# Kernel optimization log

Hardware: AMD Instinct MI355X
Metric: run time of the kernel (lower is better)

The kernel has to match this reference:

```python
import jax, jax.numpy as jnp
import numpy as np

EMBED_DIM = 1024
NUM_HEADS = 16
HEAD_DIM = EMBED_DIM // NUM_HEADS


def setup_inputs() -> dict:
    key = jax.random.key(0)
    k_x, k_wqkv, k_bqkv, k_wo, k_bo = jax.random.split(key, 5)
    B, T, C = 4, 2048, EMBED_DIM
    # PyTorch Linear default init scale ~ 1/sqrt(fan_in); use small normals
    s = 1.0 / np.sqrt(C)
    return {
        "x": jax.random.normal(k_x, (B, T, C), dtype=jnp.float32),
        "w_qkv": jax.random.normal(k_wqkv, (C, 3 * C), dtype=jnp.float32) * s,
        "b_qkv": jax.random.normal(k_bqkv, (3 * C,), dtype=jnp.float32) * s,
        "w_out": jax.random.normal(k_wo, (C, C), dtype=jnp.float32) * s,
        "b_out": jax.random.normal(k_bo, (C,), dtype=jnp.float32) * s,
    }


def reference(x, w_qkv, b_qkv, w_out, b_out):
    B, T, C = x.shape
    H, D = NUM_HEADS, HEAD_DIM
    qkv = x @ w_qkv + b_qkv                      # (B, T, 3C)
    q, k, v = jnp.split(qkv, 3, axis=-1)
    # (B, H, T, D)
    q = q.reshape(B, T, H, D).transpose(0, 2, 1, 3)
    k = k.reshape(B, T, H, D).transpose(0, 2, 1, 3)
    v = v.reshape(B, T, H, D).transpose(0, 2, 1, 3)
    scores = jnp.einsum("bhqd,bhkd->bhqk", q, k) / jnp.sqrt(jnp.float32(D))
    causal = jnp.tril(jnp.ones((T, T), dtype=bool))  # (T, T)
    scores = jnp.where(causal[None, None, :, :], scores, -jnp.inf)
    attn = jax.nn.softmax(scores, axis=-1)
    out = jnp.einsum("bhqk,bhkd->bhqd", attn, v)  # (B, H, T, D)
    out = out.transpose(0, 2, 1, 3).reshape(B, T, C)
    return out @ w_out + b_out
```

## Files before the change

### kernel.cpp

```cpp
#include <hip/hip_runtime.h>
#include <hip/hip_bf16.h>

#define B_  4
#define T_  2048
#define C_  1024
#define H_  16
#define D_  64
#define BH_ (B_*H_)

typedef float  f32x4  __attribute__((ext_vector_type(4)));
typedef __bf16 bf16x8 __attribute__((ext_vector_type(8)));
typedef __bf16 bf16x2 __attribute__((ext_vector_type(2)));

static __device__ __forceinline__ ushort f2bf(float f) {
    union { float f; unsigned u; } x; x.f = f;
    unsigned r = ((x.u >> 16) & 1u) + 0x7fffu;
    return (ushort)((x.u + r) >> 16);
}

static __device__ __forceinline__ uint packbf(float a, float b) {
    bf16x2 v = { (__bf16)a, (__bf16)b };
    return __builtin_bit_cast(uint, v);
}

static __device__ __forceinline__ void gload_lds16(const void* g, void* l) {
    __builtin_amdgcn_global_load_lds(
        (const __attribute__((address_space(1))) unsigned int*)g,
        (__attribute__((address_space(3))) unsigned int*)l, 16, 0, 0);
}

template<int N> static __device__ __forceinline__ void waitcnt_vm() {
    if constexpr (N == 0) asm volatile("s_waitcnt vmcnt(0)" ::: "memory");
    else if constexpr (N == 3) asm volatile("s_waitcnt vmcnt(3)" ::: "memory");
    else if constexpr (N == 4) asm volatile("s_waitcnt vmcnt(4)" ::: "memory");
    else static_assert(N == 0 || N == 3 || N == 4);
    __builtin_amdgcn_sched_barrier(0);
}
static __device__ __forceinline__ void lgkm0() {
    asm volatile("s_waitcnt lgkmcnt(0)" ::: "memory");
    __builtin_amdgcn_sched_barrier(0);
}

__global__ void cvt_kernel(const float* __restrict__ in, ushort* __restrict__ out, int n) {
    int i = (blockIdx.x * blockDim.x + threadIdx.x) * 4;
    if (i < n) {
        float4 v = *(const float4*)(in + i);
        ushort4 o;
        o.x = f2bf(v.x); o.y = f2bf(v.y); o.z = f2bf(v.z); o.w = f2bf(v.w);
        *(ushort4*)(out + i) = o;
    }
}

__global__ void transpose_cvt_kernel(const float* __restrict__ in, ushort* __restrict__ out,
                                     int K, int N) {
    __shared__ float tile[32][33];
    int k0 = blockIdx.y * 32, n0 = blockIdx.x * 32;
    int tx = threadIdx.x & 31, ty = threadIdx.x >> 5;
    #pragma unroll
    for (int r = 0; r < 32; r += 8)
        tile[ty + r][tx] = in[(size_t)(k0 + ty + r) * N + n0 + tx];
    __syncthreads();
    #pragma unroll
    for (int r = 0; r < 32; r += 8)
        out[(size_t)(n0 + ty + r) * K + k0 + tx] = f2bf(tile[tx][ty + r]);
}

__global__ void transpose_v_kernel(const ushort* __restrict__ v, ushort* __restrict__ vt) {
    __shared__ ushort tile[64][66];
    int bh = blockIdx.x >> 5;
    int t0 = (blockIdx.x & 31) * 64;
    const ushort* src = v  + ((size_t)bh * T_ + t0) * D_;
    ushort*       dst = vt + (size_t)bh * D_ * T_ + t0;
    int tx = threadIdx.x & 63, ty = threadIdx.x >> 6;
    #pragma unroll
    for (int r = 0; r < 64; r += 4)
        tile[ty + r][tx] = src[(size_t)(ty + r) * D_ + tx];
    __syncthreads();
    #pragma unroll
    for (int r = 0; r < 64; r += 4)
        dst[(size_t)(ty + r) * T_ + tx] = tile[tx][ty + r];
}

template<int NFR, bool QKV>
__global__ __launch_bounds__(512, 2) void gemm_hk(
    const ushort* __restrict__ A,
    const ushort* __restrict__ Bt,
    const float*  __restrict__ bias,
    void* __restrict__ outp)
{
    constexpr int NT   = 16;
    constexpr int BN   = NFR * 64;
    constexpr int ABUF = 32768;
    constexpr int BBUF = BN * 128;
    constexpr int LB   = (NFR == 4) ? 2 : 1;
    constexpr int PK   = 2 + LB;
    __shared__ __align__(16) char lds[2 * ABUF + 2 * BBUF];
    char* ldsB = lds + 2 * ABUF;

    const int m0 = blockIdx.y * 256, n0 = blockIdx.x * BN;
    const int tid = threadIdx.x, lane = tid & 63;
    const int wv = tid >> 6, wm = wv >> 2, wn = wv & 3;
    const int lr = lane & 15, lh = lane >> 4;

    const int sc = (tid & 3) ^ ((tid >> 2) & 3);
    const ushort* aA = A  + (size_t)(m0 + (tid >> 2)) * 1024 + sc * 8;
    const ushort* aB = Bt + (size_t)(n0 + (tid >> 2)) * 1024 + sc * 8;

    const int cxor = (lh ^ (lr & 3)) * 16;
    const int arow = (wm * 128 + lr) * 64 + cxor;
    const int brow = (wn * (NFR * 16) + lr) * 64 + cxor;

    f32x4 acc[8][NFR] = {};

    auto stage_a = [&](int buf, int t, int kh) {
        #pragma unroll
        for (int p = 0; p < 2; ++p)
            gload_lds16(aA + (size_t)p * 131072 + t * 64 + kh * 32,
                        lds + buf * ABUF + kh * 16384 + p * 8192 + tid * 16);
    };
    auto stage_b = [&](int buf, int t, int kh) {
        #pragma unroll
        for (int p = 0; p < LB; ++p)
            gload_lds16(aB + (size_t)p * 131072 + t * 64 + kh * 32,
                        ldsB + buf * BBUF + kh * (BBUF / 2) + p * 8192 + tid * 16);
    };
    auto read_a = [&](bf16x8 (&af)[8], int buf, int kh) {
        const char* base = lds + buf * ABUF + kh * 16384 + arow;
        #pragma unroll
        for (int mi = 0; mi < 8; ++mi) af[mi] = *(const bf16x8*)(base + mi * 1024);
    };
    auto read_b = [&](bf16x8& b0, bf16x8& b1, int buf, int kh, int nh) {
        const char* base = ldsB + buf * BBUF + kh * (BBUF / 2) + brow + nh * 2048;
        b0 = *(const bf16x8*)(base);
        b1 = *(const bf16x8*)(base + 1024);
    };

#define MFMA2(NI, BB0, BB1)                                                          \
    do {                                                                             \
        __builtin_amdgcn_s_setprio(1);                                               \
        _Pragma("unroll")                                                            \
        for (int mi = 0; mi < 8; ++mi) {                                             \
            acc[mi][NI]     = __builtin_amdgcn_mfma_f32_16x16x32_bf16(af[mi], BB0,   \
                                                     acc[mi][NI], 0, 0, 0);          \
            acc[mi][NI + 1] = __builtin_amdgcn_mfma_f32_16x16x32_bf16(af[mi], BB1,   \
                                                     acc[mi][NI + 1], 0, 0, 0);      \
        }                                                                            \
        __builtin_amdgcn_s_setprio(0);                                               \
    } while (0)

    stage_a(0, 0, 0); stage_b(0, 0, 0);
    stage_a(0, 0, 1); stage_b(0, 0, 1);
    waitcnt_vm<PK>();
    __builtin_amdgcn_s_barrier();

    for (int t = 0; t < NT; ++t) {
        const int cur = t & 1, nxt = cur ^ 1;
        const bool pf = (t + 1 < NT);
        bf16x8 af[8], b0, b1;
        if constexpr (NFR == 4) {
            read_a(af, cur, 0); read_b(b0, b1, cur, 0, 0);
            if (pf) stage_a(nxt, t + 1, 0);
            __builtin_amdgcn_s_barrier();
            lgkm0();
            MFMA2(0, b0, b1);
            read_b(b0, b1, cur, 0, 1);
            if (pf) stage_b(nxt, t + 1, 0);
            if (t < NT - 1) waitcnt_vm<4>(); else waitcnt_vm<0>();
            __builtin_amdgcn_s_barrier();
            lgkm0();
            MFMA2(2, b0, b1);
            read_a(af, cur, 1); read_b(b0, b1, cur, 1, 0);
            if (pf) stage_a(nxt, t + 1, 1);
            __builtin_amdgcn_s_barrier();
            lgkm0();
            MFMA2(0, b0, b1);
            read_b(b0, b1, cur, 1, 1);
            if (pf) stage_b(nxt, t + 1, 1);
            if (t < NT - 1) waitcnt_vm<4>();
            __builtin_amdgcn_s_barrier();
            lgkm0();
            MFMA2(2, b0, b1);
        } else {
            read_a(af, cur, 0); read_b(b0, b1, cur, 0, 0);
            if (pf) { stage_a(nxt, t + 1, 0); stage_b(nxt, t + 1, 0); }
            if (t < NT - 1) waitcnt_vm<3>(); else waitcnt_vm<0>();
            __builtin_amdgcn_s_barrier();
            lgkm0();
            MFMA2(0, b0, b1);
            read_a(af, cur, 1); read_b(b0, b1, cur, 1, 0);
            if (pf) { stage_a(nxt, t + 1, 1); stage_b(nxt, t + 1, 1); }
            if (t < NT - 1) waitcnt_vm<3>();
            __builtin_amdgcn_s_barrier();
            lgkm0();
            MFMA2(0, b0, b1);
        }
    }
#undef MFMA2

    #pragma unroll
    for (int mi = 0; mi < 8; ++mi) {
        #pragma unroll
        for (int ni = 0; ni < NFR; ++ni) {
            int col = n0 + wn * (NFR * 16) + ni * 16 + lr;
            float bv = bias[col];
            if constexpr (QKV) {
                ushort* qkv = (ushort*)outp;
                int which = col >> 10;
                int h = (col & 1023) >> 6;
                int d = col & 63;
                #pragma unroll
                for (int r = 0; r < 4; ++r) {
                    int row = m0 + wm * 128 + mi * 16 + lh * 4 + r;
                    int b = row >> 11, tt = row & 2047;
                    float v = acc[mi][ni][r] + bv;
                    if (which == 0) v *= 0.18033688011112042f;
                    qkv[(size_t)which * (BH_ * T_ * D_) +
                        (((size_t)(b * H_ + h)) * T_ + tt) * D_ + d] = f2bf(v);
                }
            } else {
                float* Cout = (float*)outp;
                #pragma unroll
                for (int r = 0; r < 4; ++r) {
                    int row = m0 + wm * 128 + mi * 16 + lh * 4 + r;
                    Cout[(size_t)row * C_ + col] = acc[mi][ni][r] + bv;
                }
            }
        }
    }
}

__global__ __launch_bounds__(256, 4) void flash_kernel(
    const ushort* __restrict__ qb,
    const ushort* __restrict__ kb,
    const ushort* __restrict__ vt,
    ushort* __restrict__ ob)
{
    __shared__ __align__(16) ushort sK[2][64 * 64];
    __shared__ __align__(16) ushort sV[2][64 * 64];
    __shared__ __align__(16) ushort sP[4][16 * 64];
    const int bh  = blockIdx.x >> 4;
    const int pr  = blockIdx.x & 15;
    const int qtA = pr, qtB = 31 - pr;
    const int lane = threadIdx.x & 63, wv = threadIdx.x >> 6;
    const int lr = lane & 15, lh = lane >> 4;

    const ushort* qrowA = qb + ((size_t)bh * T_ + qtA * 64 + wv * 16 + lr) * D_;
    const ushort* qrowB = qb + ((size_t)bh * T_ + qtB * 64 + wv * 16 + lr) * D_;
    bf16x8 qfA0 = *(const bf16x8*)(qrowA + lh * 8);
    bf16x8 qfA1 = *(const bf16x8*)(qrowA + 32 + lh * 8);
    bf16x8 qfB0 = *(const bf16x8*)(qrowB + lh * 8);
    bf16x8 qfB1 = *(const bf16x8*)(qrowB + 32 + lh * 8);

    const int srow = lane >> 3;
    const int scol = ((lane & 7) ^ srow) * 8;
    const ushort* kbase = kb + (size_t)bh * T_ * D_;
    const ushort* vbase = vt + (size_t)bh * D_ * T_;

    const int sw   = (lr & 7) << 4;
    const int off0 = (16 * lh) ^ sw;
    const int off1 = (64 + 16 * lh) ^ sw;

    f32x4 oA[4] = {}, oB[4] = {};
    float mA = -1e30f, lA = 0.f, mB = -1e30f, lB = 0.f;

    auto redmax = [&](float x) {
        x = fmaxf(x, __int_as_float(__builtin_amdgcn_ds_swizzle(__float_as_int(x), 0x401F)));
        x = fmaxf(x, __shfl_xor(x, 32, 64));
        return x;
    };
    auto redsum = [&](float x) {
        x += __int_as_float(__builtin_amdgcn_ds_swizzle(__float_as_int(x), 0x401F));
        x += __shfl_xor(x, 32, 64);
        return x;
    };

    auto tile = [&](f32x4 (&o)[4], float& mrow, float& lsum,
                    const bf16x8& q0f, const bf16x8& q1f,
                    const char* K0, const char* V0, bool diag) {
        f32x4 s[4];
        __builtin_amdgcn_s_setprio(1);
        #pragma unroll
        for (int nt = 0; nt < 4; ++nt) {
            const char* krow = K0 + (nt * 16 + lr) * 128;
            bf16x8 k0 = *(const bf16x8*)(krow + off0);
            bf16x8 k1 = *(const bf16x8*)(krow + off1);
            f32x4 a = {0.f, 0.f, 0.f, 0.f};
            a = __builtin_amdgcn_mfma_f32_16x16x32_bf16(k0, q0f, a, 0, 0, 0);
            a = __builtin_amdgcn_mfma_f32_16x16x32_bf16(k1, q1f, a, 0, 0, 0);
            s[nt] = a;
        }
        __builtin_amdgcn_s_setprio(0);
        if (diag) {
            #pragma unroll
            for (int nt = 0; nt < 4; ++nt)
                #pragma unroll
                for (int r = 0; r < 4; ++r)
                    if (nt * 16 + lh * 4 + r > wv * 16 + lr) s[nt][r] = -INFINITY;
        }

        float pmax = fmaxf(fmaxf(fmaxf(s[0][0], s[0][1]), fmaxf(s[0][2], s[0][3])),
                           fmaxf(fmaxf(s[1][0], s[1][1]), fmaxf(s[1][2], s[1][3])));
        pmax = fmaxf(pmax, fmaxf(fmaxf(fmaxf(s[2][0], s[2][1]), fmaxf(s[2][2], s[2][3])),
                                 fmaxf(fmaxf(s[3][0], s[3][1]), fmaxf(s[3][2], s[3][3]))));
        pmax = redmax(pmax);

        if (__any(pmax > mrow + 8.f)) {
            float mnew = fmaxf(mrow, pmax);
            float al = __builtin_exp2f(mrow - mnew);
            lsum *= al;
            #pragma unroll
            for (int r = 0; r < 4; ++r) {
                float ar = __shfl(al, lh * 20 + r, 64);
                o[0][r] *= ar; o[1][r] *= ar; o[2][r] *= ar; o[3][r] *= ar;
            }
            mrow = mnew;
        }

        float rsum = 0.f;
        uint pk[8];
        #pragma unroll
        for (int nt = 0; nt < 4; ++nt) {
            float p0 = __builtin_exp2f(s[nt][0] - mrow);
            float p1 = __builtin_exp2f(s[nt][1] - mrow);
            float p2 = __builtin_exp2f(s[nt][2] - mrow);
            float p3 = __builtin_exp2f(s[nt][3] - mrow);
            rsum += (p0 + p1) + (p2 + p3);
            pk[nt * 2]     = packbf(p0, p1);
            pk[nt * 2 + 1] = packbf(p2, p3);
        }
        lsum += redsum(rsum);

        char* P = (char*)sP[wv];
        {
            char* prow = P + lr * 128;
            #pragma unroll
            for (int nt = 0; nt < 4; ++nt) {
                uint2 w; w.x = pk[nt * 2]; w.y = pk[nt * 2 + 1];
                *(uint2*)(prow + ((32 * nt + 8 * lh) ^ sw)) = w;
            }
        }
        asm volatile("" ::: "memory");
        bf16x8 pf0 = *(const bf16x8*)(P + lr * 128 + off0);
        bf16x8 pf1 = *(const bf16x8*)(P + lr * 128 + off1);

        __builtin_amdgcn_s_setprio(1);
        #pragma unroll
        for (int dt = 0; dt < 4; ++dt) {
            const char* vrow = V0 + (dt * 16 + lr) * 128;
            bf16x8 v0 = *(const bf16x8*)(vrow + off0);
            bf16x8 v1 = *(const bf16x8*)(vrow + off1);
            o[dt] = __builtin_amdgcn_mfma_f32_16x16x32_bf16(pf0, v0, o[dt], 0, 0, 0);
            o[dt] = __builtin_amdgcn_mfma_f32_16x16x32_bf16(pf1, v1, o[dt], 0, 0, 0);
        }
        __builtin_amdgcn_s_setprio(0);
    };

    #pragma unroll
    for (int i = 0; i < 2; ++i) {
        int j = i * 4 + wv;
        gload_lds16(kbase + (size_t)(j * 8 + srow) * D_ + scol, &sK[0][j * 512]);
        gload_lds16(vbase + (size_t)(j * 8 + srow) * T_ + scol, &sV[0][j * 512]);
    }
    __syncthreads();

    for (int kt = 0; kt <= qtB; ++kt) {
        const int cur = kt & 1;
        if (kt < qtB) {
            const int nb = cur ^ 1;
            #pragma unroll
            for (int i = 0; i < 2; ++i) {
                int j = i * 4 + wv;
                gload_lds16(kbase + (size_t)((kt + 1) * 64 + j * 8 + srow) * D_ + scol, &sK[nb][j * 512]);
                gload_lds16(vbase + (size_t)(j * 8 + srow) * T_ + (kt + 1) * 64 + scol, &sV[nb][j * 512]);
            }
        }
        const char* K0 = (const char*)sK[cur];
        const char* V0 = (const char*)sV[cur];
        if (kt <= qtA) tile(oA, mA, lA, qfA0, qfA1, K0, V0, kt == qtA);
        tile(oB, mB, lB, qfB0, qfB1, K0, V0, kt == qtB);
        __syncthreads();
    }

    const int b = bh >> 4, h = bh & 15;
    auto writeout = [&](f32x4 (&o)[4], float lsum, int q0) {
        float inv = 1.f / lsum;
        #pragma unroll
        for (int r = 0; r < 4; ++r) {
            float ir = __shfl(inv, lh * 20 + r, 64);
            int q = q0 + lh * 4 + r;
            #pragma unroll
            for (int dt = 0; dt < 4; ++dt)
                ob[((size_t)b * T_ + q) * C_ + h * 64 + dt * 16 + lr] = f2bf(o[dt][r] * ir);
        }
    };
    writeout(oA, lA, qtA * 64 + wv * 16);
    writeout(oB, lB, qtB * 64 + wv * 16);
}

extern "C" void kernel_launch(void* const* d_in, const int* in_sizes, int n_in,
                              void* d_out, int out_size, void* d_ws, size_t ws_size,
                              hipStream_t stream) {
    const float* x     = (const float*)d_in[0];
    const float* w_qkv = (const float*)d_in[1];
    const float* b_qkv = (const float*)d_in[2];
    const float* w_out = (const float*)d_in[3];
    const float* b_out = (const float*)d_in[4];
    float* out = (float*)d_out;

    char* ws = (char*)d_ws;
    ushort* xb     = (ushort*)(ws + 0);
    ushort* wqkvT  = (ushort*)(ws + 16777216);
    ushort* woutT  = (ushort*)(ws + 23068672);
    ushort* qkv    = (ushort*)(ws + 25165824);
    ushort* vT     = (ushort*)(ws + 75497472);
    ushort* attn   = xb;
    ushort* qb = qkv;
    ushort* kb = qkv + (size_t)BH_ * T_ * D_;
    ushort* vb = qkv + (size_t)2 * BH_ * T_ * D_;

    const int nx = B_ * T_ * C_;
    cvt_kernel<<<nx / 4 / 256, 256, 0, stream>>>(x, xb, nx);
    transpose_cvt_kernel<<<dim3(3 * C_ / 32, C_ / 32), 256, 0, stream>>>(w_qkv, wqkvT, C_, 3 * C_);
    transpose_cvt_kernel<<<dim3(C_ / 32, C_ / 32), 256, 0, stream>>>(w_out, woutT, C_, C_);
    gemm_hk<4, true><<<dim3(3 * C_ / 256, B_ * T_ / 256), 512, 0, stream>>>(xb, wqkvT, b_qkv, qkv);
    transpose_v_kernel<<<BH_ * (T_ / 64), 256, 0, stream>>>(vb, vT);
    flash_kernel<<<BH_ * 16, 256, 0, stream>>>(qb, kb, vT, attn);
    gemm_hk<2, false><<<dim3(C_ / 128, B_ * T_ / 256), 512, 0, stream>>>(attn, woutT, b_out, out);
}
```

Baseline: 205.2 us.

## Store QKV in natural row-major layout and interleave A/B tiles in flash loop

The QKV GEMM epilogue now writes bf16 results row-major as (B*T, 3072) instead of scattering into a per-head (BH, T, D) layout, and it applies the Q scale as a per-block constant. The V transpose and flash kernel read Q and K directly from that layout with a 3072-element row stride. The flash kernel also splits its tile routine into QK, mask, softmax, P-write and PV stages, and issues both QK MFMA groups before either softmax so the two query tiles can overlap. This aims to get more coalesced epilogue stores and more MFMA/ALU overlap, at the cost of strided K/Q loads and higher register pressure.

```diff
diff --git a/kernel.cpp b/kernel.cpp
--- a/kernel.cpp
+++ b/kernel.cpp
@@ -65,16 +65,17 @@
         out[(size_t)(n0 + ty + r) * K + k0 + tx] = f2bf(tile[tx][ty + r]);
 }
 
-__global__ void transpose_v_kernel(const ushort* __restrict__ v, ushort* __restrict__ vt) {
+__global__ void transpose_v_kernel(const ushort* __restrict__ qkvN, ushort* __restrict__ vt) {
     __shared__ ushort tile[64][66];
     int bh = blockIdx.x >> 5;
     int t0 = (blockIdx.x & 31) * 64;
-    const ushort* src = v  + ((size_t)bh * T_ + t0) * D_;
+    int b = bh >> 4, h = bh & 15;
+    const ushort* src = qkvN + (size_t)(b * T_ + t0) * 3072 + 2048 + h * 64;
     ushort*       dst = vt + (size_t)bh * D_ * T_ + t0;
     int tx = threadIdx.x & 63, ty = threadIdx.x >> 6;
     #pragma unroll
     for (int r = 0; r < 64; r += 4)
-        tile[ty + r][tx] = src[(size_t)(ty + r) * D_ + tx];
+        tile[ty + r][tx] = src[(size_t)(ty + r) * 3072 + tx];
     __syncthreads();
     #pragma unroll
     for (int r = 0; r < 64; r += 4)
@@ -197,28 +198,30 @@
     }
 #undef MFMA2
 
-    #pragma unroll
-    for (int mi = 0; mi < 8; ++mi) {
-        #pragma unroll
-        for (int ni = 0; ni < NFR; ++ni) {
-            int col = n0 + wn * (NFR * 16) + ni * 16 + lr;
-            float bv = bias[col];
-            if constexpr (QKV) {
-                ushort* qkv = (ushort*)outp;
-                int which = col >> 10;
-                int h = (col & 1023) >> 6;
-                int d = col & 63;
+    if constexpr (QKV) {
+        ushort* qkvN = (ushort*)outp;
+        const float qs = (n0 < 1024) ? 0.18033688011112042f : 1.f;
+        #pragma unroll
+        for (int mi = 0; mi < 8; ++mi) {
+            #pragma unroll
+            for (int ni = 0; ni < NFR; ++ni) {
+                int col = n0 + wn * (NFR * 16) + ni * 16 + lr;
+                float bv = bias[col];
                 #pragma unroll
                 for (int r = 0; r < 4; ++r) {
                     int row = m0 + wm * 128 + mi * 16 + lh * 4 + r;
-                    int b = row >> 11, tt = row & 2047;
-                    float v = acc[mi][ni][r] + bv;
-                    if (which == 0) v *= 0.18033688011112042f;
-                    qkv[(size_t)which * (BH_ * T_ * D_) +
-                        (((size_t)(b * H_ + h)) * T_ + tt) * D_ + d] = f2bf(v);
+                    qkvN[(size_t)row * 3072 + col] = f2bf((acc[mi][ni][r] + bv) * qs);
                 }
-            } else {
-                float* Cout = (float*)outp;
+            }
+        }
+    } else {
+        float* Cout = (float*)outp;
+        #pragma unroll
+        for (int mi = 0; mi < 8; ++mi) {
+            #pragma unroll
+            for (int ni = 0; ni < NFR; ++ni) {
+                int col = n0 + wn * (NFR * 16) + ni * 16 + lr;
+                float bv = bias[col];
                 #pragma unroll
                 for (int r = 0; r < 4; ++r) {
                     int row = m0 + wm * 128 + mi * 16 + lh * 4 + r;
@@ -230,8 +233,7 @@
 }
 
 __global__ __launch_bounds__(256, 4) void flash_kernel(
-    const ushort* __restrict__ qb,
-    const ushort* __restrict__ kb,
+    const ushort* __restrict__ qkvN,
     const ushort* __restrict__ vt,
     ushort* __restrict__ ob)
 {
@@ -243,17 +245,20 @@
     const int qtA = pr, qtB = 31 - pr;
     const int lane = threadIdx.x & 63, wv = threadIdx.x >> 6;
     const int lr = lane & 15, lh = lane >> 4;
-
-    const ushort* qrowA = qb + ((size_t)bh * T_ + qtA * 64 + wv * 16 + lr) * D_;
-    const ushort* qrowB = qb + ((size_t)bh * T_ + qtB * 64 + wv * 16 + lr) * D_;
-    bf16x8 qfA0 = *(const bf16x8*)(qrowA + lh * 8);
-    bf16x8 qfA1 = *(const bf16x8*)(qrowA + 32 + lh * 8);
-    bf16x8 qfB0 = *(const bf16x8*)(qrowB + lh * 8);
-    bf16x8 qfB1 = *(const bf16x8*)(qrowB + 32 + lh * 8);
+    const int b = bh >> 4, h = bh & 15;
+
+    const ushort* qN = qkvN + (size_t)b * T_ * 3072 + h * 64;
+    const ushort* kN = qN + 1024;
+
+    const ushort* qrA = qN + (size_t)(qtA * 64 + wv * 16 + lr) * 3072;
+    const ushort* qrB = qN + (size_t)(qtB * 64 + wv * 16 + lr) * 3072;
+    bf16x8 qfA0 = *(const bf16x8*)(qrA + lh * 8);
+    bf16x8 qfA1 = *(const bf16x8*)(qrA + 32 + lh * 8);
+    bf16x8 qfB0 = *(const bf16x8*)(qrB + lh * 8);
+    bf16x8 qfB1 = *(const bf16x8*)(qrB + 32 + lh * 8);
 
     const int srow = lane >> 3;
     const int scol = ((lane & 7) ^ srow) * 8;
-    const ushort* kbase = kb + (size_t)bh * T_ * D_;
     const ushort* vbase = vt + (size_t)bh * D_ * T_;
 
     const int sw   = (lr & 7) << 4;
@@ -274,10 +279,7 @@
         return x;
     };
 
-    auto tile = [&](f32x4 (&o)[4], float& mrow, float& lsum,
-                    const bf16x8& q0f, const bf16x8& q1f,
-                    const char* K0, const char* V0, bool diag) {
-        f32x4 s[4];
+    auto qk = [&](f32x4 (&s)[4], const bf16x8& q0f, const bf16x8& q1f, const char* K0) {
         __builtin_amdgcn_s_setprio(1);
         #pragma unroll
         for (int nt = 0; nt < 4; ++nt) {
@@ -290,20 +292,20 @@
             s[nt] = a;
         }
         __builtin_amdgcn_s_setprio(0);
-        if (diag) {
-            #pragma unroll
-            for (int nt = 0; nt < 4; ++nt)
-                #pragma unroll
-                for (int r = 0; r < 4; ++r)
-                    if (nt * 16 + lh * 4 + r > wv * 16 + lr) s[nt][r] = -INFINITY;
-        }
-
+    };
+    auto mask = [&](f32x4 (&s)[4]) {
+        #pragma unroll
+        for (int nt = 0; nt < 4; ++nt)
+            #pragma unroll
+            for (int r = 0; r < 4; ++r)
+                if (nt * 16 + lh * 4 + r > wv * 16 + lr) s[nt][r] = -INFINITY;
+    };
+    auto smax = [&](f32x4 (&s)[4], float& mrow, float& lsum, f32x4 (&o)[4], uint (&pk)[8]) {
         float pmax = fmaxf(fmaxf(fmaxf(s[0][0], s[0][1]), fmaxf(s[0][2], s[0][3])),
                            fmaxf(fmaxf(s[1][0], s[1][1]), fmaxf(s[1][2], s[1][3])));
         pmax = fmaxf(pmax, fmaxf(fmaxf(fmaxf(s[2][0], s[2][1]), fmaxf(s[2][2], s[2][3])),
                                  fmaxf(fmaxf(s[3][0], s[3][1]), fmaxf(s[3][2], s[3][3]))));
         pmax = redmax(pmax);
-
         if (__any(pmax > mrow + 8.f)) {
             float mnew = fmaxf(mrow, pmax);
             float al = __builtin_exp2f(mrow - mnew);
@@ -315,9 +317,7 @@
             }
             mrow = mnew;
         }
-
         float rsum = 0.f;
-        uint pk[8];
         #pragma unroll
         for (int nt = 0; nt < 4; ++nt) {
             float p0 = __builtin_exp2f(s[nt][0] - mrow);
@@ -329,20 +329,18 @@
             pk[nt * 2 + 1] = packbf(p2, p3);
         }
         lsum += redsum(rsum);
-
-        char* P = (char*)sP[wv];
-        {
-            char* prow = P + lr * 128;
-            #pragma unroll
-            for (int nt = 0; nt < 4; ++nt) {
-                uint2 w; w.x = pk[nt * 2]; w.y = pk[nt * 2 + 1];
-                *(uint2*)(prow + ((32 * nt + 8 * lh) ^ sw)) = w;
-            }
-        }
-        asm volatile("" ::: "memory");
-        bf16x8 pf0 = *(const bf16x8*)(P + lr * 128 + off0);
-        bf16x8 pf1 = *(const bf16x8*)(P + lr * 128 + off1);
-
+    };
+    auto pwrite = [&](uint (&pk)[8]) {
+        char* prow = (char*)sP[wv] + lr * 128;
+        #pragma unroll
+        for (int nt = 0; nt < 4; ++nt) {
+            uint2 w; w.x = pk[nt * 2]; w.y = pk[nt * 2 + 1];
+            *(uint2*)(prow + ((32 * nt + 8 * lh) ^ sw)) = w;
+        }
+    };
+    auto pv = [&](f32x4 (&o)[4], const char* V0) {
+        bf16x8 pf0 = *(const bf16x8*)((char*)sP[wv] + lr * 128 + off0);
+        bf16x8 pf1 = *(const bf16x8*)((char*)sP[wv] + lr * 128 + off1);
         __builtin_amdgcn_s_setprio(1);
         #pragma unroll
         for (int dt = 0; dt < 4; ++dt) {
@@ -358,7 +356,7 @@
     #pragma unroll
     for (int i = 0; i < 2; ++i) {
         int j = i * 4 + wv;
-        gload_lds16(kbase + (size_t)(j * 8 + srow) * D_ + scol, &sK[0][j * 512]);
+        gload_lds16(kN + (size_t)(j * 8 + srow) * 3072 + scol, &sK[0][j * 512]);
         gload_lds16(vbase + (size_t)(j * 8 + srow) * T_ + scol, &sV[0][j * 512]);
     }
     __syncthreads();
@@ -370,18 +368,41 @@
             #pragma unroll
             for (int i = 0; i < 2; ++i) {
                 int j = i * 4 + wv;
-                gload_lds16(kbase + (size_t)((kt + 1) * 64 + j * 8 + srow) * D_ + scol, &sK[nb][j * 512]);
+                gload_lds16(kN + (size_t)((kt + 1) * 64 + j * 8 + srow) * 3072 + scol, &sK[nb][j * 512]);
                 gload_lds16(vbase + (size_t)(j * 8 + srow) * T_ + (kt + 1) * 64 + scol, &sV[nb][j * 512]);
             }
         }
+        const bool doA = kt <= qtA;
         const char* K0 = (const char*)sK[cur];
         const char* V0 = (const char*)sV[cur];
-        if (kt <= qtA) tile(oA, mA, lA, qfA0, qfA1, K0, V0, kt == qtA);
-        tile(oB, mB, lB, qfB0, qfB1, K0, V0, kt == qtB);
+
+        f32x4 sb[4];
+        uint pk[8];
+        if (doA) {
+            f32x4 sa[4];
+            qk(sb, qfB0, qfB1, K0);
+            qk(sa, qfA0, qfA1, K0);
+            if (kt == qtB) mask(sb);
+            if (kt == qtA) mask(sa);
+            smax(sa, mA, lA, oA, pk);
+            pwrite(pk);
+            asm volatile("" ::: "memory");
+            pv(oA, V0);
+            smax(sb, mB, lB, oB, pk);
+            pwrite(pk);
+            asm volatile("" ::: "memory");
+            pv(oB, V0);
+        } else {
+            qk(sb, qfB0, qfB1, K0);
+            if (kt == qtB) mask(sb);
+            smax(sb, mB, lB, oB, pk);
+            pwrite(pk);
+            asm volatile("" ::: "memory");
+            pv(oB, V0);
+        }
         __syncthreads();
     }
 
-    const int b = bh >> 4, h = bh & 15;
     auto writeout = [&](f32x4 (&o)[4], float lsum, int q0) {
         float inv = 1.f / lsum;
         #pragma unroll
@@ -411,19 +432,16 @@
     ushort* xb     = (ushort*)(ws + 0);
     ushort* wqkvT  = (ushort*)(ws + 16777216);
     ushort* woutT  = (ushort*)(ws + 23068672);
-    ushort* qkv    = (ushort*)(ws + 25165824);
+    ushort* qkvN   = (ushort*)(ws + 25165824);
     ushort* vT     = (ushort*)(ws + 75497472);
     ushort* attn   = xb;
-    ushort* qb = qkv;
-    ushort* kb = qkv + (size_t)BH_ * T_ * D_;
-    ushort* vb = qkv + (size_t)2 * BH_ * T_ * D_;
 
     const int nx = B_ * T_ * C_;
     cvt_kernel<<<nx / 4 / 256, 256, 0, stream>>>(x, xb, nx);
     transpose_cvt_kernel<<<dim3(3 * C_ / 32, C_ / 32), 256, 0, stream>>>(w_qkv, wqkvT, C_, 3 * C_);
     transpose_cvt_kernel<<<dim3(C_ / 32, C_ / 32), 256, 0, stream>>>(w_out, woutT, C_, C_);
-    gemm_hk<4, true><<<dim3(3 * C_ / 256, B_ * T_ / 256), 512, 0, stream>>>(xb, wqkvT, b_qkv, qkv);
-    transpose_v_kernel<<<BH_ * (T_ / 64), 256, 0, stream>>>(vb, vT);
-    flash_kernel<<<BH_ * 16, 256, 0, stream>>>(qb, kb, vT, attn);
+    gemm_hk<4, true><<<dim3(3 * C_ / 256, B_ * T_ / 256), 512, 0, stream>>>(xb, wqkvT, b_qkv, qkvN);
+    transpose_v_kernel<<<BH_ * (T_ / 64), 256, 0, stream>>>(qkvN, vT);
+    flash_kernel<<<BH_ * 16, 256, 0, stream>>>(qkvN, vT, attn);
     gemm_hk<2, false><<<dim3(C_ / 128, B_ * T_ / 256), 512, 0, stream>>>(attn, woutT, b_out, out);
 }
```

Measured after the change: 406.7 us. +98.2%, slower.
